# Kernel tuning notes

Hardware: AMD Instinct MI355X
Metric: run time of the kernel (lower is better)

The kernel has to match this reference:

```python
import jax, jax.numpy as jnp
import numpy as np

B, CURR, IN_DIM, H, W = 16, 256, 64, 128, 128


def setup_inputs() -> dict:
    key = jax.random.key(0)
    ks = jax.random.split(key, 11)
    s = 0.05
    return {
        "x": jax.random.normal(ks[0], (B, CURR, H, W), dtype=jnp.float32),
        "w_in": jax.random.normal(ks[1], (IN_DIM, CURR), dtype=jnp.float32) * s,
        "b_in": jax.random.normal(ks[2], (IN_DIM,), dtype=jnp.float32) * s,
        "wq": jax.random.normal(ks[3], (IN_DIM, IN_DIM), dtype=jnp.float32) * s,
        "bq": jax.random.normal(ks[4], (IN_DIM,), dtype=jnp.float32) * s,
        "wk": jax.random.normal(ks[5], (IN_DIM, IN_DIM), dtype=jnp.float32) * s,
        "bk": jax.random.normal(ks[6], (IN_DIM,), dtype=jnp.float32) * s,
        "wv": jax.random.normal(ks[7], (IN_DIM, IN_DIM), dtype=jnp.float32) * s,
        "bv": jax.random.normal(ks[8], (IN_DIM,), dtype=jnp.float32) * s,
        "w_out": jax.random.normal(ks[9], (CURR, IN_DIM), dtype=jnp.float32) * s,
        "b_out": jax.random.normal(ks[10], (CURR,), dtype=jnp.float32) * s,
    }


def reference(x, w_in, b_in, wq, bq, wk, bk, wv, bv, w_out, b_out):
    # 1x1 conv input projection: [B,curr,H,W] -> [B,C,H,W], C = input_dim
    p = jnp.einsum('bchw,oc->bohw', x, w_in) + b_in[None, :, None, None]
    b, c, h, w = p.shape
    n = h * w
    flat = p.reshape(b, c, n).transpose(0, 2, 1)  # [B,N,C]
    # Linear layers (torch: y = x @ W.T + b)
    q = flat @ wq.T + bq
    k = flat @ wk.T + bk
    v = flat @ wv.T + bv
    scale = np.float32(1.0 / np.sqrt(c))
    # channel-wise attention: score[b,i,j] = sum_n q[b,n,i] * k[b,n,j]
    score = jnp.einsum('bni,bnj->bij', q, k) * scale  # [B,C,C]
    attn = jax.nn.softmax(score, axis=2)
    # weighted = values @ attention : [B,N,C] @ [B,C,C] -> [B,N,C]
    weighted = jnp.einsum('bnc,bcj->bnj', v, attn)
    w4 = weighted.transpose(0, 2, 1).reshape(b, c, h, w)
    # 1x1 conv output projection back to curr_dim + residual
    out = jnp.einsum('bchw,oc->bohw', w4, w_out) + b_out[None, :, None, None]
    return out + x
```

## Files before the change

kernel.cpp:

```cpp
#include <hip/hip_runtime.h>

typedef unsigned short u16;
typedef __attribute__((ext_vector_type(4))) float f32x4;
typedef __attribute__((ext_vector_type(4))) unsigned int u32x4;
typedef __attribute__((ext_vector_type(2))) unsigned int u32x2;
typedef __attribute__((ext_vector_type(8))) __bf16 bf16x8;

#define NB 16
#define NC 256
#define ND 64
#define NPIX 16384

static constexpr size_t O_GX   = 0;
static constexpr size_t O_SX   = O_GX + (size_t)NB*NC*NC;
static constexpr size_t O_AQ   = O_SX + (size_t)NB*NC;
static constexpr size_t O_AKT  = O_AQ + (size_t)ND*NC;
static constexpr size_t O_AV   = O_AKT + (size_t)NC*ND;
static constexpr size_t O_BQ   = O_AV + (size_t)ND*NC;
static constexpr size_t O_BK   = O_BQ + ND;
static constexpr size_t O_BV   = O_BK + ND;
static constexpr size_t O_S1   = O_BV + ND;
static constexpr size_t O_TQ   = O_S1 + (size_t)NB*ND*NC;
static constexpr size_t O_TK   = O_TQ + (size_t)NB*ND;
static constexpr size_t O_SC   = O_TK + (size_t)NB*ND;
static constexpr size_t O_BIAS = O_SC + (size_t)NB*ND*ND;
static constexpr size_t O_GB   = O_BIAS + (size_t)NB*NC;
static constexpr size_t O_GP   = O_GB + (size_t)NB*NC*NC/2;
static constexpr size_t GP_FLOATS = (size_t)16*NB*NC*NC;

__device__ __forceinline__ int fsw(int row) { return ((row ^ (row >> 3)) & 7) << 4; }

__device__ __forceinline__ u16 f2bf(float f) {
  union { float f; unsigned u; } v; v.f = f;
  unsigned r = v.u + 0x7fffu + ((v.u >> 16) & 1u);
  return (u16)(r >> 16);
}

__global__ void k0_weights(const float* __restrict__ w_in, const float* __restrict__ b_in,
                           const float* __restrict__ wq, const float* __restrict__ bqv,
                           const float* __restrict__ wk, const float* __restrict__ bkv,
                           const float* __restrict__ wv, const float* __restrict__ bvv,
                           float* __restrict__ ws) {
  const int m = blockIdx.x >> 2, cc = blockIdx.x & 3;
  const float* w = (m == 0) ? wq : (m == 1) ? wk : wv;
  const int t = threadIdx.x;
  const int i = t >> 2;
  const int c0 = cc*64 + (t & 3)*16;
  float acc[16];
  #pragma unroll
  for (int e = 0; e < 16; ++e) acc[e] = 0.f;
  for (int j = 0; j < 64; ++j) {
    const float wij = w[i*64 + j];
    const float* wr = w_in + (size_t)j*NC + c0;
    #pragma unroll
    for (int e = 0; e < 16; ++e) acc[e] += wij * wr[e];
  }
  if (m == 0)      { float* A = ws + O_AQ;  for (int e = 0; e < 16; ++e) A[(size_t)i*NC + c0 + e] = acc[e]; }
  else if (m == 1) { float* A = ws + O_AKT; for (int e = 0; e < 16; ++e) A[(size_t)(c0+e)*ND + i] = acc[e]; }
  else             { float* A = ws + O_AV;  for (int e = 0; e < 16; ++e) A[(size_t)i*NC + c0 + e] = acc[e]; }
  if (cc == 0 && t < 64) {
    float a = 0.f;
    for (int j = 0; j < 64; ++j) a += w[t*64 + j] * b_in[j];
    a += ((m == 0) ? bqv : (m == 1) ? bkv : bvv)[t];
    ws[((m == 0) ? O_BQ : (m == 1) ? O_BK : O_BV) + t] = a;
  }
}

template<bool PART>
__global__ __launch_bounds__(512, 2) void k1_gram(const float* __restrict__ x, float* __restrict__ ws) {
  const int b = blockIdx.x & 15, ks = blockIdx.x >> 4;
  const float* xb = x + (size_t)b*NC*NPIX + (size_t)ks*1024;
  __shared__ u16 lds[2][NC*64];
  const int t = threadIdx.x, lane = t & 63, wid = t >> 6;
  const int wr = wid >> 1, wc = wid & 1;
  const int srow = t >> 2, scol = (t & 3) * 16;
  const f32x4 vzero = {0.f, 0.f, 0.f, 0.f};

  f32x4 pf[2][4];
  float csum[2] = {0.f, 0.f};
  f32x4 acc[4][8];
  #pragma unroll
  for (int i2 = 0; i2 < 4; ++i2)
    #pragma unroll
    for (int j2 = 0; j2 < 8; ++j2) acc[i2][j2] = vzero;

  auto load_iter = [&](int it) {
    #pragma unroll
    for (int p = 0; p < 2; ++p) {
      const float* src = xb + (size_t)(srow + p*128)*NPIX + it*64 + scol;
      #pragma unroll
      for (int j = 0; j < 4; ++j) pf[p][j] = *(const f32x4*)(src + j*4);
    }
  };
  auto store_iter = [&](int buf) {
    char* base = (char*)&lds[buf][0];
    #pragma unroll
    for (int p = 0; p < 2; ++p) {
      const int row = srow + p*128;
      const int fb = fsw(row);
      u16 h[16];
      float s = 0.f;
      #pragma unroll
      for (int j = 0; j < 4; ++j)
        #pragma unroll
        for (int e = 0; e < 4; ++e) { const float v = pf[p][j][e]; s += v; h[j*4+e] = f2bf(v); }
      csum[p] += s;
      u32x4 w0, w1;
      #pragma unroll
      for (int q = 0; q < 4; ++q) w0[q] = (unsigned)h[2*q]   | ((unsigned)h[2*q+1]   << 16);
      #pragma unroll
      for (int q = 0; q < 4; ++q) w1[q] = (unsigned)h[8+2*q] | ((unsigned)h[8+2*q+1] << 16);
      *(u32x4*)(base + row*128 + ((scol*2)      ^ fb)) = w0;
      *(u32x4*)(base + row*128 + ((scol*2 + 16) ^ fb)) = w1;
    }
  };

  load_iter(0);
  store_iter(0);
  __syncthreads();
  for (int it = 0; it < 16; ++it) {
    const int cur = it & 1;
    if (it < 15) load_iter(it + 1);
    const char* base = (const char*)&lds[cur][0];
    #pragma unroll
    for (int kk = 0; kk < 2; ++kk) {
      const int kb = kk*64 + (lane >> 4) * 16;
      bf16x8 af[4], bfv[8];
      #pragma unroll
      for (int mi = 0; mi < 4; ++mi) {
        const int row = wr*64 + mi*16 + (lane & 15);
        af[mi] = *(const bf16x8*)(base + row*128 + (kb ^ fsw(row)));
      }
      #pragma unroll
      for (int ni = 0; ni < 8; ++ni) {
        const int row = wc*128 + ni*16 + (lane & 15);
        bfv[ni] = *(const bf16x8*)(base + row*128 + (kb ^ fsw(row)));
      }
      #pragma unroll
      for (int mi = 0; mi < 4; ++mi)
        #pragma unroll
        for (int ni = 0; ni < 8; ++ni)
          acc[mi][ni] = __builtin_amdgcn_mfma_f32_16x16x32_bf16(af[mi], bfv[ni], acc[mi][ni], 0, 0, 0);
    }
    if (it < 15) store_iter(cur ^ 1);
    __syncthreads();
  }

  #pragma unroll
  for (int p = 0; p < 2; ++p) {
    float s = csum[p];
    s += __shfl_xor(s, 1);
    s += __shfl_xor(s, 2);
    if ((t & 3) == 0) atomicAdd(ws + O_SX + b*NC + srow + p*128, s);
  }

  if (PART) {
    float* dst = ws + O_GP + ((size_t)ks*NB + b)*((size_t)NC*NC);
    #pragma unroll
    for (int mi = 0; mi < 4; ++mi)
      #pragma unroll
      for (int ni = 0; ni < 8; ++ni)
        #pragma unroll
        for (int e = 0; e < 4; ++e) {
          const int rr = wr*64 + mi*16 + (lane >> 4)*4 + e;
          const int dd = wc*128 + ni*16 + (lane & 15);
          dst[(size_t)rr*NC + dd] = acc[mi][ni][e];
        }
  } else {
    float* dst = ws + O_GX + (size_t)b*NC*NC;
    #pragma unroll
    for (int mi = 0; mi < 4; ++mi)
      #pragma unroll
      for (int ni = 0; ni < 8; ++ni)
        #pragma unroll
        for (int e = 0; e < 4; ++e) {
          const int rr = wr*64 + mi*16 + (lane >> 4)*4 + e;
          const int dd = wc*128 + ni*16 + (lane & 15);
          atomicAdd(dst + (size_t)rr*NC + dd, acc[mi][ni][e]);
        }
  }
}

__global__ void k1_reduce(float* __restrict__ ws) {
  const size_t idx = ((size_t)blockIdx.x * 256 + threadIdx.x) * 4;
  const f32x4 vzero = {0.f, 0.f, 0.f, 0.f};
  f32x4 a = vzero;
  #pragma unroll
  for (int ks = 0; ks < 16; ++ks)
    a += *(const f32x4*)(ws + O_GP + (size_t)ks*NB*NC*NC + idx);
  *(f32x4*)(ws + O_GX + idx) = a;
}

__global__ void k2_s1(float* __restrict__ ws) {
  const int b = blockIdx.x >> 2, jc = blockIdx.x & 3;
  const int t = threadIdx.x;
  const int i = t >> 3, j0 = jc*64 + (t & 7)*8;
  const float* Gx = ws + O_GX + (size_t)b*NC*NC;
  const float* Aq = ws + O_AQ;
  const f32x4 vzero = {0.f, 0.f, 0.f, 0.f};
  f32x4 a0 = vzero, a1 = vzero;
  for (int c = 0; c < 256; ++c) {
    const float a = Aq[(size_t)i*NC + c];
    const float* g = Gx + (size_t)c*NC + j0;
    a0 += a * *(const f32x4*)(g);
    a1 += a * *(const f32x4*)(g + 4);
  }
  float* s1 = ws + O_S1 + (size_t)b*ND*NC + (size_t)i*NC + j0;
  *(f32x4*)(s1) = a0; *(f32x4*)(s1 + 4) = a1;
  if (jc == 0 && t < 128) {
    const float* sxp = ws + O_SX + b*NC;
    float a = 0.f;
    if (t < 64) {
      for (int c = 0; c < 256; ++c) a += ws[O_AKT + (size_t)c*ND + t] * sxp[c];
      ws[O_TK + b*ND + t] = a;
    } else {
      const int i2 = t - 64;
      for (int c = 0; c < 256; ++c) a += ws[O_AQ + (size_t)i2*NC + c] * sxp[c];
      ws[O_TQ + b*ND + i2] = a;
    }
  }
}

__global__ void k2_score(float* __restrict__ ws) {
  const int b = blockIdx.x >> 2, jc = blockIdx.x & 3;
  const int t = threadIdx.x;
  const int i = t >> 3, j = jc*16 + (t & 7)*2;
  const float* s1 = ws + O_S1 + (size_t)b*ND*NC + (size_t)i*NC;
  const float* akt = ws + O_AKT;
  float a0 = 0.f, a1 = 0.f;
  for (int d = 0; d < 256; ++d) {
    const float s = s1[d];
    a0 += s * akt[(size_t)d*ND + j];
    a1 += s * akt[(size_t)d*ND + j + 1];
  }
  const float bq = ws[O_BQ + i], tq = ws[O_TQ + b*ND + i];
  const float bk0 = ws[O_BK + j], bk1 = ws[O_BK + j + 1];
  const float tk0 = ws[O_TK + b*ND + j], tk1 = ws[O_TK + b*ND + j + 1];
  const float sc = 0.125f;
  float* so = ws + O_SC + (size_t)b*ND*ND + (size_t)i*ND + j;
  so[0] = sc*(a0 + bq*tk0 + tq*bk0 + 16384.f*bq*bk0);
  so[1] = sc*(a1 + bq*tk1 + tq*bk1 + 16384.f*bq*bk1);
}

__global__ void k2_attn_g(const float* __restrict__ w_out, const float* __restrict__ b_out,
                          float* __restrict__ ws) {
  const int b = blockIdx.x >> 2, oc = blockIdx.x & 3;
  const int t = threadIdx.x;
  __shared__ float sc[64*68];
  __shared__ float at[64*68];
  __shared__ float ml[64*68];
  #pragma unroll
  for (int k = 0; k < 8; ++k) {
    const int idx = t + k*512;
    sc[(idx >> 6)*68 + (idx & 63)] = ws[O_SC + (size_t)b*ND*ND + idx];
  }
  __syncthreads();
  if (t < 64) {
    float m = -1e30f;
    for (int j = 0; j < 64; ++j) m = fmaxf(m, sc[t*68 + j]);
    float s = 0.f;
    for (int j = 0; j < 64; ++j) { const float e = __expf(sc[t*68 + j] - m); sc[t*68 + j] = e; s += e; }
    const float inv = 1.f / s;
    for (int j = 0; j < 64; ++j) at[j*68 + t] = sc[t*68 + j] * inv;
  }
  __syncthreads();
  {
    const int o = t >> 3, c0 = (t & 7)*8;
    float acc[8];
    #pragma unroll
    for (int e = 0; e < 8; ++e) acc[e] = 0.f;
    for (int j = 0; j < 64; ++j) {
      const float w = w_out[(size_t)(oc*64 + o)*ND + j];
      #pragma unroll
      for (int e = 0; e < 8; ++e) acc[e] += w * at[j*68 + c0 + e];
    }
    #pragma unroll
    for (int e = 0; e < 8; ++e) ml[o*68 + c0 + e] = acc[e];
  }
  __syncthreads();
  {
    const int c0 = (t & 15)*16;
    #pragma unroll
    for (int or2 = 0; or2 < 2; ++or2) {
      const int o = (t >> 4) + or2*32;
      float acc[16];
      #pragma unroll
      for (int e = 0; e < 16; ++e) acc[e] = 0.f;
      for (int c = 0; c < 64; ++c) {
        const float m = ml[o*68 + c];
        const float* av = ws + O_AV + (size_t)c*NC + c0;
        #pragma unroll
        for (int e = 0; e < 16; ++e) acc[e] += m * av[e];
      }
      u16* gb = (u16*)(ws + O_GB) + (size_t)b*NC*NC + (size_t)(oc*64 + o)*NC + c0;
      u16 h[16];
      #pragma unroll
      for (int e = 0; e < 16; ++e) h[e] = f2bf(acc[e]);
      u32x4 w0, w1;
      #pragma unroll
      for (int q = 0; q < 4; ++q) w0[q] = (unsigned)h[2*q]   | ((unsigned)h[2*q+1]   << 16);
      #pragma unroll
      for (int q = 0; q < 4; ++q) w1[q] = (unsigned)h[8+2*q] | ((unsigned)h[8+2*q+1] << 16);
      *(u32x4*)(gb) = w0;
      *(u32x4*)(gb + 8) = w1;
    }
  }
  if (t < 64) {
    float a = 0.f;
    for (int c = 0; c < 64; ++c) a += ml[t*68 + c] * ws[O_BV + c];
    ws[O_BIAS + b*NC + oc*64 + t] = a + b_out[oc*64 + t];
  }
}

__global__ __launch_bounds__(512, 2) void k3_apply(const float* __restrict__ x,
                                                   const float* __restrict__ ws,
                                                   float* __restrict__ out) {
  const int wg = (blockIdx.x & 7) * 128 + (blockIdx.x >> 3);
  const int b = wg >> 6, nt = wg & 63;
  const float* xb = x + (size_t)b*NC*NPIX + (size_t)nt*256;
  const u16* Gb = (const u16*)(ws + O_GB) + (size_t)b*NC*NC;
  const int t = threadIdx.x, lane = t & 63, wid = t >> 6;
  const int wr = wid >> 1, wc = wid & 1;

  __shared__ __align__(16) unsigned char smem[132096];
  float* bias_lds = (float*)(smem + 131072);
  if (t < 256) bias_lds[t] = ws[O_BIAS + b*NC + t];

  const f32x4 vzero = {0.f, 0.f, 0.f, 0.f};
  u32x4 pa[4];
  f32x4 pb[2][4];
  f32x4 acc[4][8];
  #pragma unroll
  for (int i2 = 0; i2 < 4; ++i2)
    #pragma unroll
    for (int j2 = 0; j2 < 8; ++j2) acc[i2][j2] = vzero;

  auto loadA = [&](int s) {
    const u16* src = Gb + (size_t)(t >> 1)*NC + s*64 + (t & 1)*32;
    #pragma unroll
    for (int j = 0; j < 4; ++j) pa[j] = *(const u32x4*)(src + j*8);
  };
  auto loadB = [&](int s) {
    #pragma unroll
    for (int g = 0; g < 2; ++g) {
      const int id = t + g*512, mc = id >> 6, mn = id & 63;
      const float* src = xb + (size_t)(s*64 + mc*4)*NPIX + mn*4;
      #pragma unroll
      for (int i = 0; i < 4; ++i) pb[g][i] = *(const f32x4*)(src + (size_t)i*NPIX);
    }
  };
  auto storeA = [&](int buf) {
    char* base = (char*)smem + buf*65536;
    const int row = t >> 1, fb = fsw(row);
    #pragma unroll
    for (int j = 0; j < 4; ++j)
      *(u32x4*)(base + row*128 + ((((t & 1)*64) + j*16) ^ fb)) = pa[j];
  };
  auto storeB = [&](int buf) {
    char* base = (char*)smem + buf*65536 + 32768;
    #pragma unroll
    for (int g = 0; g < 2; ++g) {
      const int id = t + g*512, mc = id >> 6, mn = id & 63;
      #pragma unroll
      for (int j = 0; j < 4; ++j) {
        const int row = mn*4 + j;
        u32x2 val;
        val[0] = (unsigned)f2bf(pb[g][0][j]) | ((unsigned)f2bf(pb[g][1][j]) << 16);
        val[1] = (unsigned)f2bf(pb[g][2][j]) | ((unsigned)f2bf(pb[g][3][j]) << 16);
        *(u32x2*)(base + row*128 + ((mc*8) ^ fsw(row))) = val;
      }
    }
  };

  loadA(0); loadB(0);
  storeA(0); storeB(0);
  __syncthreads();
  for (int s = 0; s < 4; ++s) {
    const int cur = s & 1;
    if (s < 3) { loadA(s + 1); loadB(s + 1); }
    const char* Ab = (const char*)smem + cur*65536;
    const char* Bb = (const char*)smem + cur*65536 + 32768;
    #pragma unroll
    for (int kk = 0; kk < 2; ++kk) {
      const int kb = kk*64 + (lane >> 4)*16;
      bf16x8 af[4], bfv[8];
      #pragma unroll
      for (int mi = 0; mi < 4; ++mi) {
        const int row = wr*64 + mi*16 + (lane & 15);
        af[mi] = *(const bf16x8*)(Ab + row*128 + (kb ^ fsw(row)));
      }
      #pragma unroll
      for (int ni = 0; ni < 8; ++ni) {
        const int row = wc*128 + ni*16 + (lane & 15);
        bfv[ni] = *(const bf16x8*)(Bb + row*128 + (kb ^ fsw(row)));
      }
      #pragma unroll
      for (int mi = 0; mi < 4; ++mi)
        #pragma unroll
        for (int ni = 0; ni < 8; ++ni)
          acc[mi][ni] = __builtin_amdgcn_mfma_f32_16x16x32_bf16(af[mi], bfv[ni], acc[mi][ni], 0, 0, 0);
    }
    if (s < 3) { storeA(cur ^ 1); storeB(cur ^ 1); }
    __syncthreads();
  }

  float* ep = (float*)smem + wid * (16*132);
  const size_t obase = (size_t)b*NC*NPIX + (size_t)nt*256 + wc*128;
  #pragma unroll
  for (int mi = 0; mi < 4; ++mi) {
    #pragma unroll
    for (int ni = 0; ni < 8; ++ni)
      #pragma unroll
      for (int e = 0; e < 4; ++e)
        ep[((lane >> 4)*4 + e)*132 + ni*16 + (lane & 15)] = acc[mi][ni][e];
    asm volatile("s_waitcnt lgkmcnt(0)" ::: "memory");
    const int o = wr*64 + mi*16 + (lane & 15);
    const float bo = bias_lds[o];
    const float* resp = x + obase + (size_t)o*NPIX + (lane >> 4)*32;
    float* op = out + obase + (size_t)o*NPIX + (lane >> 4)*32;
    #pragma unroll
    for (int j = 0; j < 8; ++j) {
      f32x4 v = *(const f32x4*)(ep + (lane & 15)*132 + (lane >> 4)*32 + j*4);
      const f32x4 r = *(const f32x4*)(resp + j*4);
      v = v + r + bo;
      *(f32x4*)(op + j*4) = v;
    }
  }
}

extern "C" void kernel_launch(void* const* d_in, const int* in_sizes, int n_in,
                              void* d_out, int out_size, void* d_ws, size_t ws_size,
                              hipStream_t stream) {
  const float* x     = (const float*)d_in[0];
  const float* w_in  = (const float*)d_in[1];
  const float* b_in  = (const float*)d_in[2];
  const float* wq    = (const float*)d_in[3];
  const float* bq    = (const float*)d_in[4];
  const float* wk    = (const float*)d_in[5];
  const float* bk    = (const float*)d_in[6];
  const float* wv    = (const float*)d_in[7];
  const float* bv    = (const float*)d_in[8];
  const float* w_out = (const float*)d_in[9];
  const float* b_out = (const float*)d_in[10];
  float* out = (float*)d_out;
  float* ws  = (float*)d_ws;

  hipMemsetAsync(ws, 0, O_AQ * sizeof(float), stream);
  k0_weights<<<12, 256, 0, stream>>>(w_in, b_in, wq, bq, wk, bk, wv, bv, ws);

  const bool part = ws_size >= (O_GP + GP_FLOATS) * sizeof(float);
  if (part) {
    k1_gram<true><<<256, 512, 0, stream>>>(x, ws);
    k1_reduce<<<1024, 256, 0, stream>>>(ws);
  } else {
    k1_gram<false><<<256, 512, 0, stream>>>(x, ws);
  }
  k2_s1<<<64, 512, 0, stream>>>(ws);
  k2_score<<<64, 512, 0, stream>>>(ws);
  k2_attn_g<<<64, 512, 0, stream>>>(w_out, b_out, ws);
  k3_apply<<<1024, 512, 0, stream>>>(x, ws, out);
}
```

Measured before the change: 832.8 us.

## Split Gram and apply kernels into smaller tiles with more blocks

The Gram kernel now launches twice as many blocks, each computing half of the output columns, and drops LDS double-buffering in favour of a single buffer with higher occupancy. The apply kernel switches to 256-thread blocks over 64-pixel tiles, reads the G matrix directly from global memory instead of staging it in LDS, and writes outputs straight from the accumulators without an LDS transpose. The memset is narrowed to the column-sum region when the partial-buffer path is used. The aim is more parallelism and latency hiding through occupancy. The cost is redundant x loads and bf16 conversion across the two halves, lost load/compute overlap, and scalar, less coalesced epilogue stores.

```diff
diff --git a/kernel.cpp b/kernel.cpp
--- a/kernel.cpp
+++ b/kernel.cpp
@@ -67,91 +67,82 @@
 }
 
 template<bool PART>
-__global__ __launch_bounds__(512, 2) void k1_gram(const float* __restrict__ x, float* __restrict__ ws) {
-  const int b = blockIdx.x & 15, ks = blockIdx.x >> 4;
+__global__ __launch_bounds__(512, 4) void k1_gram(const float* __restrict__ x, float* __restrict__ ws) {
+  const int bid = blockIdx.x;
+  const int q = bid >> 4, r = bid & 15;
+  const int pair = q*8 + (r & 7), half = r >> 3;
+  const int b = pair >> 4, ks = pair & 15;
   const float* xb = x + (size_t)b*NC*NPIX + (size_t)ks*1024;
-  __shared__ u16 lds[2][NC*64];
+
+  __shared__ __align__(16) u16 tl[NC*64];
   const int t = threadIdx.x, lane = t & 63, wid = t >> 6;
   const int wr = wid >> 1, wc = wid & 1;
-  const int srow = t >> 2, scol = (t & 3) * 16;
+  const int srow = t >> 2, spx = (t & 3) * 16;
+
   const f32x4 vzero = {0.f, 0.f, 0.f, 0.f};
-
-  f32x4 pf[2][4];
+  f32x4 acc[4][4];
+  #pragma unroll
+  for (int i2 = 0; i2 < 4; ++i2)
+    #pragma unroll
+    for (int j2 = 0; j2 < 4; ++j2) acc[i2][j2] = vzero;
   float csum[2] = {0.f, 0.f};
-  f32x4 acc[4][8];
-  #pragma unroll
-  for (int i2 = 0; i2 < 4; ++i2)
-    #pragma unroll
-    for (int j2 = 0; j2 < 8; ++j2) acc[i2][j2] = vzero;
-
-  auto load_iter = [&](int it) {
-    #pragma unroll
-    for (int p = 0; p < 2; ++p) {
-      const float* src = xb + (size_t)(srow + p*128)*NPIX + it*64 + scol;
-      #pragma unroll
-      for (int j = 0; j < 4; ++j) pf[p][j] = *(const f32x4*)(src + j*4);
-    }
-  };
-  auto store_iter = [&](int buf) {
-    char* base = (char*)&lds[buf][0];
-    #pragma unroll
-    for (int p = 0; p < 2; ++p) {
-      const int row = srow + p*128;
+
+  for (int it = 0; it < 16; ++it) {
+    __syncthreads();
+    #pragma unroll
+    for (int g = 0; g < 2; ++g) {
+      const int row = srow + g*128;
+      const float* src = xb + (size_t)row*NPIX + it*64 + spx;
+      f32x4 ld[4];
+      #pragma unroll
+      for (int j = 0; j < 4; ++j) ld[j] = *(const f32x4*)(src + j*4);
+      u16 h[16]; float s = 0.f;
+      #pragma unroll
+      for (int j = 0; j < 4; ++j)
+        #pragma unroll
+        for (int e = 0; e < 4; ++e) { const float v = ld[j][e]; s += v; h[j*4+e] = f2bf(v); }
+      csum[g] += s;
+      u32x4 w0, w1;
+      #pragma unroll
+      for (int p = 0; p < 4; ++p) w0[p] = (unsigned)h[2*p]   | ((unsigned)h[2*p+1]   << 16);
+      #pragma unroll
+      for (int p = 0; p < 4; ++p) w1[p] = (unsigned)h[8+2*p] | ((unsigned)h[8+2*p+1] << 16);
+      char* base = (char*)tl + row*128;
       const int fb = fsw(row);
-      u16 h[16];
-      float s = 0.f;
-      #pragma unroll
-      for (int j = 0; j < 4; ++j)
-        #pragma unroll
-        for (int e = 0; e < 4; ++e) { const float v = pf[p][j][e]; s += v; h[j*4+e] = f2bf(v); }
-      csum[p] += s;
-      u32x4 w0, w1;
-      #pragma unroll
-      for (int q = 0; q < 4; ++q) w0[q] = (unsigned)h[2*q]   | ((unsigned)h[2*q+1]   << 16);
-      #pragma unroll
-      for (int q = 0; q < 4; ++q) w1[q] = (unsigned)h[8+2*q] | ((unsigned)h[8+2*q+1] << 16);
-      *(u32x4*)(base + row*128 + ((scol*2)      ^ fb)) = w0;
-      *(u32x4*)(base + row*128 + ((scol*2 + 16) ^ fb)) = w1;
-    }
-  };
-
-  load_iter(0);
-  store_iter(0);
-  __syncthreads();
-  for (int it = 0; it < 16; ++it) {
-    const int cur = it & 1;
-    if (it < 15) load_iter(it + 1);
-    const char* base = (const char*)&lds[cur][0];
+      *(u32x4*)(base + ((spx*2)      ^ fb)) = w0;
+      *(u32x4*)(base + ((spx*2 + 16) ^ fb)) = w1;
+    }
+    __syncthreads();
     #pragma unroll
     for (int kk = 0; kk < 2; ++kk) {
-      const int kb = kk*64 + (lane >> 4) * 16;
-      bf16x8 af[4], bfv[8];
+      const int kb = kk*64 + (lane >> 4)*16;
+      bf16x8 af[4], bv[4];
       #pragma unroll
       for (int mi = 0; mi < 4; ++mi) {
         const int row = wr*64 + mi*16 + (lane & 15);
-        af[mi] = *(const bf16x8*)(base + row*128 + (kb ^ fsw(row)));
-      }
-      #pragma unroll
-      for (int ni = 0; ni < 8; ++ni) {
-        const int row = wc*128 + ni*16 + (lane & 15);
-        bfv[ni] = *(const bf16x8*)(base + row*128 + (kb ^ fsw(row)));
+        af[mi] = *(const bf16x8*)((const char*)tl + row*128 + (kb ^ fsw(row)));
+      }
+      #pragma unroll
+      for (int ni = 0; ni < 4; ++ni) {
+        const int row = half*128 + wc*64 + ni*16 + (lane & 15);
+        bv[ni] = *(const bf16x8*)((const char*)tl + row*128 + (kb ^ fsw(row)));
       }
       #pragma unroll
       for (int mi = 0; mi < 4; ++mi)
         #pragma unroll
-        for (int ni = 0; ni < 8; ++ni)
-          acc[mi][ni] = __builtin_amdgcn_mfma_f32_16x16x32_bf16(af[mi], bfv[ni], acc[mi][ni], 0, 0, 0);
-    }
-    if (it < 15) store_iter(cur ^ 1);
-    __syncthreads();
-  }
-
-  #pragma unroll
-  for (int p = 0; p < 2; ++p) {
-    float s = csum[p];
-    s += __shfl_xor(s, 1);
-    s += __shfl_xor(s, 2);
-    if ((t & 3) == 0) atomicAdd(ws + O_SX + b*NC + srow + p*128, s);
+        for (int ni = 0; ni < 4; ++ni)
+          acc[mi][ni] = __builtin_amdgcn_mfma_f32_16x16x32_bf16(af[mi], bv[ni], acc[mi][ni], 0, 0, 0);
+    }
+  }
+
+  if (half == 0) {
+    #pragma unroll
+    for (int g = 0; g < 2; ++g) {
+      float s = csum[g];
+      s += __shfl_xor(s, 1);
+      s += __shfl_xor(s, 2);
+      if ((t & 3) == 0) atomicAdd(ws + O_SX + b*NC + srow + g*128, s);
+    }
   }
 
   if (PART) {
@@ -159,11 +150,11 @@
     #pragma unroll
     for (int mi = 0; mi < 4; ++mi)
       #pragma unroll
-      for (int ni = 0; ni < 8; ++ni)
+      for (int ni = 0; ni < 4; ++ni)
         #pragma unroll
         for (int e = 0; e < 4; ++e) {
           const int rr = wr*64 + mi*16 + (lane >> 4)*4 + e;
-          const int dd = wc*128 + ni*16 + (lane & 15);
+          const int dd = half*128 + wc*64 + ni*16 + (lane & 15);
           dst[(size_t)rr*NC + dd] = acc[mi][ni][e];
         }
   } else {
@@ -171,11 +162,11 @@
     #pragma unroll
     for (int mi = 0; mi < 4; ++mi)
       #pragma unroll
-      for (int ni = 0; ni < 8; ++ni)
+      for (int ni = 0; ni < 4; ++ni)
         #pragma unroll
         for (int e = 0; e < 4; ++e) {
           const int rr = wr*64 + mi*16 + (lane >> 4)*4 + e;
-          const int dd = wc*128 + ni*16 + (lane & 15);
+          const int dd = half*128 + wc*64 + ni*16 + (lane & 15);
           atomicAdd(dst + (size_t)rr*NC + dd, acc[mi][ni][e]);
         }
   }
@@ -298,9 +289,9 @@
       for (int e = 0; e < 16; ++e) h[e] = f2bf(acc[e]);
       u32x4 w0, w1;
       #pragma unroll
-      for (int q = 0; q < 4; ++q) w0[q] = (unsigned)h[2*q]   | ((unsigned)h[2*q+1]   << 16);
-      #pragma unroll
-      for (int q = 0; q < 4; ++q) w1[q] = (unsigned)h[8+2*q] | ((unsigned)h[8+2*q+1] << 16);
+      for (int p = 0; p < 4; ++p) w0[p] = (unsigned)h[2*p]   | ((unsigned)h[2*p+1]   << 16);
+      #pragma unroll
+      for (int p = 0; p < 4; ++p) w1[p] = (unsigned)h[8+2*p] | ((unsigned)h[8+2*p+1] << 16);
       *(u32x4*)(gb) = w0;
       *(u32x4*)(gb + 8) = w1;
     }
@@ -312,118 +303,80 @@
   }
 }
 
-__global__ __launch_bounds__(512, 2) void k3_apply(const float* __restrict__ x,
+__global__ __launch_bounds__(256, 4) void k3_apply(const float* __restrict__ x,
                                                    const float* __restrict__ ws,
                                                    float* __restrict__ out) {
-  const int wg = (blockIdx.x & 7) * 128 + (blockIdx.x >> 3);
-  const int b = wg >> 6, nt = wg & 63;
-  const float* xb = x + (size_t)b*NC*NPIX + (size_t)nt*256;
+  const int bid = blockIdx.x;
+  const int b = bid >> 8, nt = bid & 255;
+  const float* xb = x + (size_t)b*NC*NPIX + (size_t)nt*64;
   const u16* Gb = (const u16*)(ws + O_GB) + (size_t)b*NC*NC;
-  const int t = threadIdx.x, lane = t & 63, wid = t >> 6;
-  const int wr = wid >> 1, wc = wid & 1;
-
-  __shared__ __align__(16) unsigned char smem[132096];
-  float* bias_lds = (float*)(smem + 131072);
-  if (t < 256) bias_lds[t] = ws[O_BIAS + b*NC + t];
+  const int t = threadIdx.x, lane = t & 63, w = t >> 6;
+
+  __shared__ __align__(16) u16 blds[64*64];
+  __shared__ float bias_lds[256];
+  bias_lds[t] = ws[O_BIAS + b*NC + t];
 
   const f32x4 vzero = {0.f, 0.f, 0.f, 0.f};
-  u32x4 pa[4];
-  f32x4 pb[2][4];
-  f32x4 acc[4][8];
+  f32x4 acc[4][4];
   #pragma unroll
   for (int i2 = 0; i2 < 4; ++i2)
     #pragma unroll
-    for (int j2 = 0; j2 < 8; ++j2) acc[i2][j2] = vzero;
-
-  auto loadA = [&](int s) {
-    const u16* src = Gb + (size_t)(t >> 1)*NC + s*64 + (t & 1)*32;
-    #pragma unroll
-    for (int j = 0; j < 4; ++j) pa[j] = *(const u32x4*)(src + j*8);
-  };
-  auto loadB = [&](int s) {
-    #pragma unroll
-    for (int g = 0; g < 2; ++g) {
-      const int id = t + g*512, mc = id >> 6, mn = id & 63;
-      const float* src = xb + (size_t)(s*64 + mc*4)*NPIX + mn*4;
-      #pragma unroll
-      for (int i = 0; i < 4; ++i) pb[g][i] = *(const f32x4*)(src + (size_t)i*NPIX);
-    }
-  };
-  auto storeA = [&](int buf) {
-    char* base = (char*)smem + buf*65536;
-    const int row = t >> 1, fb = fsw(row);
-    #pragma unroll
-    for (int j = 0; j < 4; ++j)
-      *(u32x4*)(base + row*128 + ((((t & 1)*64) + j*16) ^ fb)) = pa[j];
-  };
-  auto storeB = [&](int buf) {
-    char* base = (char*)smem + buf*65536 + 32768;
-    #pragma unroll
-    for (int g = 0; g < 2; ++g) {
-      const int id = t + g*512, mc = id >> 6, mn = id & 63;
-      #pragma unroll
-      for (int j = 0; j < 4; ++j) {
-        const int row = mn*4 + j;
-        u32x2 val;
-        val[0] = (unsigned)f2bf(pb[g][0][j]) | ((unsigned)f2bf(pb[g][1][j]) << 16);
-        val[1] = (unsigned)f2bf(pb[g][2][j]) | ((unsigned)f2bf(pb[g][3][j]) << 16);
-        *(u32x2*)(base + row*128 + ((mc*8) ^ fsw(row))) = val;
-      }
-    }
-  };
-
-  loadA(0); loadB(0);
-  storeA(0); storeB(0);
-  __syncthreads();
+    for (int j2 = 0; j2 < 4; ++j2) acc[i2][j2] = vzero;
+
   for (int s = 0; s < 4; ++s) {
-    const int cur = s & 1;
-    if (s < 3) { loadA(s + 1); loadB(s + 1); }
-    const char* Ab = (const char*)smem + cur*65536;
-    const char* Bb = (const char*)smem + cur*65536 + 32768;
+    {
+      const int c0 = (t >> 4)*4, px0 = (t & 15)*4;
+      f32x4 ld[4];
+      #pragma unroll
+      for (int j = 0; j < 4; ++j)
+        ld[j] = *(const f32x4*)(xb + (size_t)(s*64 + c0 + j)*NPIX + px0);
+      __syncthreads();
+      #pragma unroll
+      for (int p = 0; p < 4; ++p) {
+        const int row = px0 + p;
+        u32x2 v;
+        v[0] = (unsigned)f2bf(ld[0][p]) | ((unsigned)f2bf(ld[1][p]) << 16);
+        v[1] = (unsigned)f2bf(ld[2][p]) | ((unsigned)f2bf(ld[3][p]) << 16);
+        *(u32x2*)((char*)blds + row*128 + ((c0*2) ^ fsw(row))) = v;
+      }
+      __syncthreads();
+    }
     #pragma unroll
     for (int kk = 0; kk < 2; ++kk) {
-      const int kb = kk*64 + (lane >> 4)*16;
-      bf16x8 af[4], bfv[8];
+      bf16x8 af[4], bv[4];
       #pragma unroll
       for (int mi = 0; mi < 4; ++mi) {
-        const int row = wr*64 + mi*16 + (lane & 15);
-        af[mi] = *(const bf16x8*)(Ab + row*128 + (kb ^ fsw(row)));
-      }
-      #pragma unroll
-      for (int ni = 0; ni < 8; ++ni) {
-        const int row = wc*128 + ni*16 + (lane & 15);
-        bfv[ni] = *(const bf16x8*)(Bb + row*128 + (kb ^ fsw(row)));
+        const int row = w*64 + mi*16 + (lane & 15);
+        af[mi] = *(const bf16x8*)(Gb + (size_t)row*NC + s*64 + kk*32 + (lane >> 4)*8);
+      }
+      #pragma unroll
+      for (int ni = 0; ni < 4; ++ni) {
+        const int row = ni*16 + (lane & 15);
+        bv[ni] = *(const bf16x8*)((const char*)blds + row*128 + ((kk*64 + (lane >> 4)*16) ^ fsw(row)));
       }
       #pragma unroll
       for (int mi = 0; mi < 4; ++mi)
         #pragma unroll
-        for (int ni = 0; ni < 8; ++ni)
-          acc[mi][ni] = __builtin_amdgcn_mfma_f32_16x16x32_bf16(af[mi], bfv[ni], acc[mi][ni], 0, 0, 0);
-    }
-    if (s < 3) { storeA(cur ^ 1); storeB(cur ^ 1); }
-    __syncthreads();
-  }
-
-  float* ep = (float*)smem + wid * (16*132);
-  const size_t obase = (size_t)b*NC*NPIX + (size_t)nt*256 + wc*128;
+        for (int ni = 0; ni < 4; ++ni)
+          acc[mi][ni] = __builtin_amdgcn_mfma_f32_16x16x32_bf16(af[mi], bv[ni], acc[mi][ni], 0, 0, 0);
+    }
+  }
+
+  const size_t colbase = (size_t)b*NC*NPIX + (size_t)nt*64;
   #pragma unroll
   for (int mi = 0; mi < 4; ++mi) {
-    #pragma unroll
-    for (int ni = 0; ni < 8; ++ni)
-      #pragma unroll
-      for (int e = 0; e < 4; ++e)
-        ep[((lane >> 4)*4 + e)*132 + ni*16 + (lane & 15)] = acc[mi][ni][e];
-    asm volatile("s_waitcnt lgkmcnt(0)" ::: "memory");
-    const int o = wr*64 + mi*16 + (lane & 15);
-    const float bo = bias_lds[o];
-    const float* resp = x + obase + (size_t)o*NPIX + (lane >> 4)*32;
-    float* op = out + obase + (size_t)o*NPIX + (lane >> 4)*32;
-    #pragma unroll
-    for (int j = 0; j < 8; ++j) {
-      f32x4 v = *(const f32x4*)(ep + (lane & 15)*132 + (lane >> 4)*32 + j*4);
-      const f32x4 r = *(const f32x4*)(resp + j*4);
-      v = v + r + bo;
-      *(f32x4*)(op + j*4) = v;
+    float bo[4];
+    #pragma unroll
+    for (int e = 0; e < 4; ++e) bo[e] = bias_lds[w*64 + mi*16 + (lane >> 4)*4 + e];
+    #pragma unroll
+    for (int ni = 0; ni < 4; ++ni) {
+      const int n = ni*16 + (lane & 15);
+      #pragma unroll
+      for (int e = 0; e < 4; ++e) {
+        const int o = w*64 + mi*16 + (lane >> 4)*4 + e;
+        const size_t a = colbase + (size_t)o*NPIX + n;
+        out[a] = acc[mi][ni][e] + bo[e] + x[a];
+      }
     }
   }
 }
@@ -445,18 +398,22 @@
   float* out = (float*)d_out;
   float* ws  = (float*)d_ws;
 
-  hipMemsetAsync(ws, 0, O_AQ * sizeof(float), stream);
-  k0_weights<<<12, 256, 0, stream>>>(w_in, b_in, wq, bq, wk, bk, wv, bv, ws);
-
   const bool part = ws_size >= (O_GP + GP_FLOATS) * sizeof(float);
   if (part) {
-    k1_gram<true><<<256, 512, 0, stream>>>(x, ws);
+    hipMemsetAsync(ws + O_SX, 0, (size_t)NB*NC*sizeof(float), stream);
+  } else {
+    hipMemsetAsync(ws, 0, O_AQ * sizeof(float), stream);
+  }
+  k0_weights<<<12, 256, 0, stream>>>(w_in, b_in, wq, bq, wk, bk, wv, bv, ws);
+
+  if (part) {
+    k1_gram<true><<<512, 512, 0, stream>>>(x, ws);
     k1_reduce<<<1024, 256, 0, stream>>>(ws);
   } else {
-    k1_gram<false><<<256, 512, 0, stream>>>(x, ws);
+    k1_gram<false><<<512, 512, 0, stream>>>(x, ws);
   }
   k2_s1<<<64, 512, 0, stream>>>(ws);
   k2_score<<<64, 512, 0, stream>>>(ws);
   k2_attn_g<<<64, 512, 0, stream>>>(w_out, b_out, ws);
-  k3_apply<<<1024, 512, 0, stream>>>(x, ws, out);
-}
+  k3_apply<<<4096, 256, 0, stream>>>(x, ws, out);
+}
```

Result: faster. 809.6 us (-2.8%).
